# Performance work log

Measured on AMD Instinct MI355X. Metric: run time of the kernel, lower is better.

The kernel has to match this reference:

```python
import jax, jax.numpy as jnp
import numpy as np

SHIFT = 1
EPS = 1e-5

def setup_inputs() -> dict:
    key = jax.random.key(0)
    k1, k2, k3, k4, k5, k6 = jax.random.split(key, 6)
    B, C, H, Wd = 64, 512, 28, 28
    Cout = 512
    return {
        "x": jax.random.normal(k1, (B, C, H, Wd), dtype=jnp.float32),
        "W": jax.random.normal(k2, (Cout, C), dtype=jnp.float32) * 0.05,
        "gamma": jax.random.uniform(k3, (Cout,), dtype=jnp.float32) + 0.5,
        "beta": jax.random.normal(k4, (Cout,), dtype=jnp.float32) * 0.1,
        "running_mean": jax.random.normal(k5, (Cout,), dtype=jnp.float32) * 0.1,
        "running_var": jax.random.uniform(k6, (Cout,), dtype=jnp.float32) + 0.5,
    }

def reference(x, W, gamma, beta, running_mean, running_var):
    # Group-wise spatial shift: split channels into 4 groups, roll each.
    Cg = x.shape[1] // 4
    x1 = jnp.roll(x[:, 0*Cg:1*Cg], -SHIFT, axis=2)  # up
    x2 = jnp.roll(x[:, 1*Cg:2*Cg],  SHIFT, axis=2)  # down
    x3 = jnp.roll(x[:, 2*Cg:3*Cg], -SHIFT, axis=3)  # left
    x4 = jnp.roll(x[:, 3*Cg:4*Cg],  SHIFT, axis=3)  # right
    shifted = jnp.concatenate([x1, x2, x3, x4], axis=1)  # [B,C,H,W]
    # 1x1 conv (no bias) == channel matmul
    y = jnp.einsum('bchw,oc->bohw', shifted, W)
    # BatchNorm (inference: running stats) folded to scale/shift, then ReLU
    scale = gamma * jax.lax.rsqrt(running_var + EPS)
    shift = beta - running_mean * scale
    y = y * scale[None, :, None, None] + shift[None, :, None, None]
    return jnp.maximum(y, 0.0)
```

## Files before the change

kernel.cpp:

```cpp
#include <hip/hip_runtime.h>

#define BN   64
#define CIN  512
#define COUT 512
#define HW   784
#define NT   128
#define MT   112
#define BK   64
#define NKB  (CIN / BK)

typedef __attribute__((ext_vector_type(8))) short short8;
typedef __attribute__((ext_vector_type(4))) float f32x4;

__device__ __forceinline__ unsigned short f2bf(float f) {
    union { float f; unsigned int u; } v; v.f = f;
    unsigned int r = v.u + 0x7fffu + ((v.u >> 16) & 1u);
    return (unsigned short)(r >> 16);
}

__device__ __forceinline__ uint2 pack4(float a, float b, float c, float d) {
    uint2 r;
    r.x = (unsigned int)f2bf(a) | ((unsigned int)f2bf(b) << 16);
    r.y = (unsigned int)f2bf(c) | ((unsigned int)f2bf(d) << 16);
    return r;
}

__global__ __launch_bounds__(256)
void p0_wcvt(const float* __restrict__ W, unsigned short* __restrict__ Wb)
{
    int gi = blockIdx.x * 256 + threadIdx.x;
    const float* p = W + (size_t)gi * 8;
    float4 a = *(const float4*)p;
    float4 c = *(const float4*)(p + 4);
    uint2 lo = pack4(a.x, a.y, a.z, a.w);
    uint2 hi = pack4(c.x, c.y, c.z, c.w);
    uint4 v; v.x = lo.x; v.y = lo.y; v.z = hi.x; v.w = hi.y;
    *(uint4*)(Wb + (size_t)gi * 8) = v;
}

__global__ __launch_bounds__(512, 2)
void p_fused(const float* __restrict__ x, const unsigned short* __restrict__ Wb,
             const float* __restrict__ gamma, const float* __restrict__ beta,
             const float* __restrict__ rmean, const float* __restrict__ rvar,
             float* __restrict__ out)
{
    __shared__ unsigned short sX[2][MT * BK];

    const int t  = threadIdx.x;
    const int id = blockIdx.x;
    const int mt = id % 7;
    const int b  = id / 7;
    const int hw_base = mt * MT;
    const int lane = t & 63, wv = t >> 6, m16 = lane & 15, q = lane >> 4;
    const float* xb = x + (size_t)b * CIN * HW;

    const int cq = t & 15;
    const int mq = t >> 4;
    const bool act = (mq < 28);
    const int hw = hw_base + mq * 4;
    const int h  = hw / 28;
    const int w0 = hw - h * 28;

    float4 va0, va1, va2, va3;
    float  ex0, ex1, ex2, ex3;

    auto loadx = [&](int kk) {
        if (!act) return;
        const int g = kk >> 1;
        const float* src = xb + (size_t)(kk * BK + cq * 4) * HW;
        if (g < 2) {
            int shw = hw + (g == 0 ? 28 : HW - 28);
            if (shw >= HW) shw -= HW;
            va0 = *(const float4*)(src + 0 * HW + shw);
            va1 = *(const float4*)(src + 1 * HW + shw);
            va2 = *(const float4*)(src + 2 * HW + shw);
            va3 = *(const float4*)(src + 3 * HW + shw);
        } else {
            const int base = h * 28;
            const int wx = (g == 2) ? ((w0 + 4 < 28) ? (w0 + 4) : 0)
                                    : ((w0 == 0) ? 27 : (w0 - 1));
            const float* r0 = src + 0 * HW + base;
            const float* r1 = src + 1 * HW + base;
            const float* r2 = src + 2 * HW + base;
            const float* r3 = src + 3 * HW + base;
            va0 = *(const float4*)(r0 + w0);  ex0 = r0[wx];
            va1 = *(const float4*)(r1 + w0);  ex1 = r1[wx];
            va2 = *(const float4*)(r2 + w0);  ex2 = r2[wx];
            va3 = *(const float4*)(r3 + w0);  ex3 = r3[wx];
        }
    };

    auto packst = [&](int kk, unsigned short* buf) {
        if (!act) return;
        const int g = kk >> 1;
        float4 r0 = va0, r1 = va1, r2 = va2, r3 = va3;
        if (g == 2) {
            r0 = make_float4(va0.y, va0.z, va0.w, ex0);
            r1 = make_float4(va1.y, va1.z, va1.w, ex1);
            r2 = make_float4(va2.y, va2.z, va2.w, ex2);
            r3 = make_float4(va3.y, va3.z, va3.w, ex3);
        } else if (g == 3) {
            r0 = make_float4(ex0, va0.x, va0.y, va0.z);
            r1 = make_float4(ex1, va1.x, va1.y, va1.z);
            r2 = make_float4(ex2, va2.x, va2.y, va2.z);
            r3 = make_float4(ex3, va3.x, va3.y, va3.z);
        }
        uint2 u0 = pack4(r0.x, r1.x, r2.x, r3.x);
        uint2 u1 = pack4(r0.y, r1.y, r2.y, r3.y);
        uint2 u2 = pack4(r0.z, r1.z, r2.z, r3.z);
        uint2 u3 = pack4(r0.w, r1.w, r2.w, r3.w);
        const int m0 = mq * 4;
        const int gr = cq >> 1, hf4 = (cq & 1) * 4;
        *(uint2*)(&buf[(m0 + 0) * BK + ((gr ^ ((m0 + 0) & 7)) * 8) + hf4]) = u0;
        *(uint2*)(&buf[(m0 + 1) * BK + ((gr ^ ((m0 + 1) & 7)) * 8) + hf4]) = u1;
        *(uint2*)(&buf[(m0 + 2) * BK + ((gr ^ ((m0 + 2) & 7)) * 8) + hf4]) = u2;
        *(uint2*)(&buf[(m0 + 3) * BK + ((gr ^ ((m0 + 3) & 7)) * 8) + hf4]) = u3;
    };

    const unsigned short* wr0 = Wb + (size_t)(wv * 64 + m16) * CIN + q * 8;
    const unsigned short* wr1 = wr0 + 16 * CIN;
    const unsigned short* wr2 = wr0 + 32 * CIN;
    const unsigned short* wr3 = wr0 + 48 * CIN;

    short8 wc[2][4], wn[2][4];
#define LOADW(DST, KK)                                  \
    {   const int ko = (KK) * 64;                       \
        DST[0][0] = *(const short8*)(wr0 + ko);         \
        DST[0][1] = *(const short8*)(wr1 + ko);         \
        DST[0][2] = *(const short8*)(wr2 + ko);         \
        DST[0][3] = *(const short8*)(wr3 + ko);         \
        DST[1][0] = *(const short8*)(wr0 + ko + 32);    \
        DST[1][1] = *(const short8*)(wr1 + ko + 32);    \
        DST[1][2] = *(const short8*)(wr2 + ko + 32);    \
        DST[1][3] = *(const short8*)(wr3 + ko + 32);    \
    }

    f32x4 acc[4][7];
    #pragma unroll
    for (int i = 0; i < 4; ++i)
        #pragma unroll
        for (int j = 0; j < 7; ++j)
            acc[i][j] = (f32x4){0.f, 0.f, 0.f, 0.f};

#define COMPUTE(XS, WF)                                                          \
    {                                                                            \
        const unsigned short* xs = (XS);                                         \
        _Pragma("unroll")                                                        \
        for (int ks = 0; ks < 2; ++ks) {                                         \
            _Pragma("unroll")                                                    \
            for (int bm = 0; bm < 7; ++bm) {                                     \
                int m  = bm * 16 + m16;                                          \
                int sl = (ks * 4 + q) ^ (m & 7);                                 \
                short8 bf = *(const short8*)(&xs[m * BK + sl * 8]);              \
                acc[0][bm] = __builtin_amdgcn_mfma_f32_16x16x32_bf16(WF[ks][0], bf, acc[0][bm], 0, 0, 0); \
                acc[1][bm] = __builtin_amdgcn_mfma_f32_16x16x32_bf16(WF[ks][1], bf, acc[1][bm], 0, 0, 0); \
                acc[2][bm] = __builtin_amdgcn_mfma_f32_16x16x32_bf16(WF[ks][2], bf, acc[2][bm], 0, 0, 0); \
                acc[3][bm] = __builtin_amdgcn_mfma_f32_16x16x32_bf16(WF[ks][3], bf, acc[3][bm], 0, 0, 0); \
            }                                                                    \
        }                                                                        \
    }

    loadx(0);
    LOADW(wc, 0);
    packst(0, sX[0]);
    __syncthreads();

    #pragma unroll 1
    for (int kp = 0; kp < 4; ++kp) {
        {
            const int kn = 2 * kp + 1;
            loadx(kn);
            LOADW(wn, kn);
            COMPUTE(sX[0], wc);
            packst(kn, sX[1]);
            __syncthreads();
        }
        {
            const int kn = 2 * kp + 2;
            if (kn < NKB) {
                loadx(kn);
                LOADW(wc, kn);
            }
            COMPUTE(sX[1], wn);
            if (kn < NKB) {
                packst(kn, sX[0]);
            }
            __syncthreads();
        }
    }
#undef COMPUTE
#undef LOADW

    float scl[4][4], shf[4][4];
    #pragma unroll
    for (int bo = 0; bo < 4; ++bo)
        #pragma unroll
        for (int r = 0; r < 4; ++r) {
            int o = wv * 64 + bo * 16 + q * 4 + r;
            float sc = gamma[o] * rsqrtf(rvar[o] + 1e-5f);
            scl[bo][r] = sc;
            shf[bo][r] = beta[o] - rmean[o] * sc;
        }
    float* outb = out + (size_t)b * COUT * HW;
    #pragma unroll
    for (int bo = 0; bo < 4; ++bo) {
        #pragma unroll
        for (int r = 0; r < 4; ++r) {
            int o = wv * 64 + bo * 16 + q * 4 + r;
            float* orow = outb + (size_t)o * HW + hw_base + m16;
            #pragma unroll
            for (int bm = 0; bm < 7; ++bm) {
                float y = acc[bo][bm][r] * scl[bo][r] + shf[bo][r];
                y = fmaxf(y, 0.f);
                __builtin_nontemporal_store(y, orow + bm * 16);
            }
        }
    }
}

#define SW_STRIDE 72
#define SX_STRIDE 64
__global__ __launch_bounds__(256, 2)
void shiftconv_fallback(const float* __restrict__ x, const float* __restrict__ Wf,
                        const float* __restrict__ gamma, const float* __restrict__ beta,
                        const float* __restrict__ rmean, const float* __restrict__ rvar,
                        float* __restrict__ out)
{
    __shared__ unsigned short sW[NT * SW_STRIDE];
    __shared__ unsigned short sX[MT * SX_STRIDE];
    const int t = threadIdx.x;
    const int ot = blockIdx.x, mt = blockIdx.y, b = blockIdx.z;
    const int o_base = ot * NT, hw_base = mt * MT;
    const float* xb = x + (size_t)b * CIN * HW;
    const int lane = t & 63, wv = t >> 6, m16 = lane & 15, q = lane >> 4;
    f32x4 acc[2][7];
    #pragma unroll
    for (int i = 0; i < 2; ++i)
        #pragma unroll
        for (int j = 0; j < 7; ++j) acc[i][j] = (f32x4){0.f, 0.f, 0.f, 0.f};
    #pragma unroll
    for (int kk = 0; kk < CIN / BK; ++kk) {
        const int k0 = kk * BK;
        const int g = k0 >> 7;
        #pragma unroll
        for (int e0 = 0; e0 < 2; ++e0) {
            int e = t + e0 * 256;
            if (e < (BK / 4) * (MT / 4)) {
                int cq = e / 28, mq = e - cq * 28;
                int hw = hw_base + mq * 4;
                const float* src = xb + (size_t)(k0 + cq * 4) * HW;
                float4 v0, v1, v2, v3;
                if (g < 2) {
                    int shw = hw + (g == 0 ? 28 : HW - 28);
                    if (shw >= HW) shw -= HW;
                    v0 = *(const float4*)(src + 0 * HW + shw);
                    v1 = *(const float4*)(src + 1 * HW + shw);
                    v2 = *(const float4*)(src + 2 * HW + shw);
                    v3 = *(const float4*)(src + 3 * HW + shw);
                } else {
                    int h = hw / 28, w0 = hw - h * 28, base = h * 28;
                    #pragma unroll
                    for (int j = 0; j < 4; ++j) {
                        const float* row = src + j * HW + base;
                        float4 a = *(const float4*)(row + w0);
                        float4 r;
                        if (g == 2) {
                            float ex = row[(w0 + 4 < 28) ? (w0 + 4) : 0];
                            r.x = a.y; r.y = a.z; r.z = a.w; r.w = ex;
                        } else {
                            float ex = row[(w0 == 0) ? 27 : (w0 - 1)];
                            r.x = ex; r.y = a.x; r.z = a.y; r.w = a.z;
                        }
                        if (j == 0) v0 = r; else if (j == 1) v1 = r;
                        else if (j == 2) v2 = r; else v3 = r;
                    }
                }
                int m0 = mq * 4;
                { int p = (cq + 5 * (m0 + 0)) & 15;
                  *(uint2*)(&sX[(m0 + 0) * SX_STRIDE + p * 4]) = pack4(v0.x, v1.x, v2.x, v3.x); }
                { int p = (cq + 5 * (m0 + 1)) & 15;
                  *(uint2*)(&sX[(m0 + 1) * SX_STRIDE + p * 4]) = pack4(v0.y, v1.y, v2.y, v3.y); }
                { int p = (cq + 5 * (m0 + 2)) & 15;
                  *(uint2*)(&sX[(m0 + 2) * SX_STRIDE + p * 4]) = pack4(v0.z, v1.z, v2.z, v3.z); }
                { int p = (cq + 5 * (m0 + 3)) & 15;
                  *(uint2*)(&sX[(m0 + 3) * SX_STRIDE + p * 4]) = pack4(v0.w, v1.w, v2.w, v3.w); }
            }
        }
        #pragma unroll
        for (int i = 0; i < 4; ++i) {
            int e = t + i * 256;
            int ol = e >> 3, kg = (e & 7) * 8;
            const float* wr = Wf + (size_t)(o_base + ol) * CIN + k0 + kg;
            float4 a = *(const float4*)(wr);
            float4 c = *(const float4*)(wr + 4);
            uint2 lo = pack4(a.x, a.y, a.z, a.w);
            uint2 hi = pack4(c.x, c.y, c.z, c.w);
            uint4 v; v.x = lo.x; v.y = lo.y; v.z = hi.x; v.w = hi.y;
            *(uint4*)(&sW[ol * SW_STRIDE + kg]) = v;
        }
        __syncthreads();
        #pragma unroll
        for (int ks = 0; ks < BK; ks += 32) {
            short8 afrag[2];
            #pragma unroll
            for (int bo = 0; bo < 2; ++bo) {
                int row = wv * 32 + bo * 16 + m16;
                afrag[bo] = *(const short8*)(&sW[row * SW_STRIDE + ks + q * 8]);
            }
            #pragma unroll
            for (int bm = 0; bm < 7; ++bm) {
                int m = bm * 16 + m16;
                int g0 = (ks >> 2) + 2 * q;
                int p0 = (g0 + 5 * m) & 15;
                int p1 = (g0 + 1 + 5 * m) & 15;
                uint2 lo = *(const uint2*)(&sX[m * SX_STRIDE + p0 * 4]);
                uint2 hi = *(const uint2*)(&sX[m * SX_STRIDE + p1 * 4]);
                union { uint2 u2[2]; short8 s; } fb;
                fb.u2[0] = lo; fb.u2[1] = hi;
                acc[0][bm] = __builtin_amdgcn_mfma_f32_16x16x32_bf16(afrag[0], fb.s, acc[0][bm], 0, 0, 0);
                acc[1][bm] = __builtin_amdgcn_mfma_f32_16x16x32_bf16(afrag[1], fb.s, acc[1][bm], 0, 0, 0);
            }
        }
        __syncthreads();
    }
    float scl[2][4], shf[2][4];
    #pragma unroll
    for (int bo = 0; bo < 2; ++bo)
        #pragma unroll
        for (int r = 0; r < 4; ++r) {
            int o = o_base + wv * 32 + bo * 16 + q * 4 + r;
            float sc = gamma[o] * rsqrtf(rvar[o] + 1e-5f);
            scl[bo][r] = sc;
            shf[bo][r] = beta[o] - rmean[o] * sc;
        }
    float* outb = out + (size_t)b * COUT * HW;
    #pragma unroll
    for (int bo = 0; bo < 2; ++bo)
        #pragma unroll
        for (int r = 0; r < 4; ++r) {
            int o = o_base + wv * 32 + bo * 16 + q * 4 + r;
            float* orow = outb + (size_t)o * HW + hw_base + m16;
            #pragma unroll
            for (int bm = 0; bm < 7; ++bm) {
                float y = acc[bo][bm][r] * scl[bo][r] + shf[bo][r];
                y = fmaxf(y, 0.f);
                __builtin_nontemporal_store(y, orow + bm * 16);
            }
        }
}

extern "C" void kernel_launch(void* const* d_in, const int* in_sizes, int n_in,
                              void* d_out, int out_size, void* d_ws, size_t ws_size,
                              hipStream_t stream)
{
    const float* x     = (const float*)d_in[0];
    const float* W     = (const float*)d_in[1];
    const float* gamma = (const float*)d_in[2];
    const float* beta  = (const float*)d_in[3];
    const float* rmean = (const float*)d_in[4];
    const float* rvar  = (const float*)d_in[5];
    float* out = (float*)d_out;

    const size_t wb_bytes = (size_t)COUT * CIN * 2;
    if (ws_size >= wb_bytes) {
        unsigned short* Wb = (unsigned short*)d_ws;
        p0_wcvt<<<dim3(128), dim3(256), 0, stream>>>(W, Wb);
        p_fused<<<dim3(448), dim3(512), 0, stream>>>(x, Wb, gamma, beta, rmean, rvar, out);
    } else {
        dim3 grid(COUT / NT, HW / MT, BN);
        shiftconv_fallback<<<grid, 256, 0, stream>>>(x, W, gamma, beta, rmean, rvar, out);
    }
}
```

Baseline: 237.2 us.

## Split output channels across 4 blocks with 256 threads for more occupancy

Each block now computes a 128-output-channel slice instead of all 512, with 256 threads per block and a 1792-block grid. Block IDs are swizzled so the four channel-tile blocks of one (batch, spatial) pair launch adjacently and can share the x tile in L2. Each thread now loads two x row groups, and the per-wave accumulator footprint halves, which allows 3 blocks per CU. The cost is that the shifted x tile is loaded from global memory and converted to bf16 four times instead of once.

```diff
diff --git a/kernel.cpp b/kernel.cpp
--- a/kernel.cpp
+++ b/kernel.cpp
@@ -38,7 +38,9 @@
     *(uint4*)(Wb + (size_t)gi * 8) = v;
 }
 
-__global__ __launch_bounds__(512, 2)
+struct XR { float4 v0, v1, v2, v3; float e0, e1, e2, e3; };
+
+__global__ __launch_bounds__(256, 3)
 void p_fused(const float* __restrict__ x, const unsigned short* __restrict__ Wb,
              const float* __restrict__ gamma, const float* __restrict__ beta,
              const float* __restrict__ rmean, const float* __restrict__ rvar,
@@ -47,34 +49,37 @@
     __shared__ unsigned short sX[2][MT * BK];
 
     const int t  = threadIdx.x;
-    const int id = blockIdx.x;
-    const int mt = id % 7;
-    const int b  = id / 7;
+    const int id   = blockIdx.x;
+    const int ot   = (id >> 3) & 3;
+    const int pair = ((id >> 5) << 3) | (id & 7);
+    const int mt   = pair % 7;
+    const int b    = pair / 7;
+    const int o_base  = ot * NT;
     const int hw_base = mt * MT;
     const int lane = t & 63, wv = t >> 6, m16 = lane & 15, q = lane >> 4;
     const float* xb = x + (size_t)b * CIN * HW;
 
-    const int cq = t & 15;
-    const int mq = t >> 4;
-    const bool act = (mq < 28);
-    const int hw = hw_base + mq * 4;
-    const int h  = hw / 28;
-    const int w0 = hw - h * 28;
-
-    float4 va0, va1, va2, va3;
-    float  ex0, ex1, ex2, ex3;
-
-    auto loadx = [&](int kk) {
-        if (!act) return;
+    const int cq  = t & 15;
+    const int mqA = t >> 4;
+    const int mqB = mqA + 16;
+    const bool actB = (mqB < 28);
+    const int hwA = hw_base + mqA * 4;
+    const int hA  = hwA / 28,  wA = hwA - hA * 28;
+    const int hwB = hw_base + mqB * 4;
+    const int hB  = hwB / 28,  wB = hwB - hB * 28;
+
+    XR ra, rb;
+
+    auto loadx = [&](int kk, int hw, int h, int w0, XR& r) {
         const int g = kk >> 1;
         const float* src = xb + (size_t)(kk * BK + cq * 4) * HW;
         if (g < 2) {
             int shw = hw + (g == 0 ? 28 : HW - 28);
             if (shw >= HW) shw -= HW;
-            va0 = *(const float4*)(src + 0 * HW + shw);
-            va1 = *(const float4*)(src + 1 * HW + shw);
-            va2 = *(const float4*)(src + 2 * HW + shw);
-            va3 = *(const float4*)(src + 3 * HW + shw);
+            r.v0 = *(const float4*)(src + 0 * HW + shw);
+            r.v1 = *(const float4*)(src + 1 * HW + shw);
+            r.v2 = *(const float4*)(src + 2 * HW + shw);
+            r.v3 = *(const float4*)(src + 3 * HW + shw);
         } else {
             const int base = h * 28;
             const int wx = (g == 2) ? ((w0 + 4 < 28) ? (w0 + 4) : 0)
@@ -83,27 +88,26 @@
             const float* r1 = src + 1 * HW + base;
             const float* r2 = src + 2 * HW + base;
             const float* r3 = src + 3 * HW + base;
-            va0 = *(const float4*)(r0 + w0);  ex0 = r0[wx];
-            va1 = *(const float4*)(r1 + w0);  ex1 = r1[wx];
-            va2 = *(const float4*)(r2 + w0);  ex2 = r2[wx];
-            va3 = *(const float4*)(r3 + w0);  ex3 = r3[wx];
+            r.v0 = *(const float4*)(r0 + w0);  r.e0 = r0[wx];
+            r.v1 = *(const float4*)(r1 + w0);  r.e1 = r1[wx];
+            r.v2 = *(const float4*)(r2 + w0);  r.e2 = r2[wx];
+            r.v3 = *(const float4*)(r3 + w0);  r.e3 = r3[wx];
         }
     };
 
-    auto packst = [&](int kk, unsigned short* buf) {
-        if (!act) return;
+    auto packst = [&](int kk, int mq, const XR& r, unsigned short* buf) {
         const int g = kk >> 1;
-        float4 r0 = va0, r1 = va1, r2 = va2, r3 = va3;
+        float4 r0 = r.v0, r1 = r.v1, r2 = r.v2, r3 = r.v3;
         if (g == 2) {
-            r0 = make_float4(va0.y, va0.z, va0.w, ex0);
-            r1 = make_float4(va1.y, va1.z, va1.w, ex1);
-            r2 = make_float4(va2.y, va2.z, va2.w, ex2);
-            r3 = make_float4(va3.y, va3.z, va3.w, ex3);
+            r0 = make_float4(r.v0.y, r.v0.z, r.v0.w, r.e0);
+            r1 = make_float4(r.v1.y, r.v1.z, r.v1.w, r.e1);
+            r2 = make_float4(r.v2.y, r.v2.z, r.v2.w, r.e2);
+            r3 = make_float4(r.v3.y, r.v3.z, r.v3.w, r.e3);
         } else if (g == 3) {
-            r0 = make_float4(ex0, va0.x, va0.y, va0.z);
-            r1 = make_float4(ex1, va1.x, va1.y, va1.z);
-            r2 = make_float4(ex2, va2.x, va2.y, va2.z);
-            r3 = make_float4(ex3, va3.x, va3.y, va3.z);
+            r0 = make_float4(r.e0, r.v0.x, r.v0.y, r.v0.z);
+            r1 = make_float4(r.e1, r.v1.x, r.v1.y, r.v1.z);
+            r2 = make_float4(r.e2, r.v2.x, r.v2.y, r.v2.z);
+            r3 = make_float4(r.e3, r.v3.x, r.v3.y, r.v3.z);
         }
         uint2 u0 = pack4(r0.x, r1.x, r2.x, r3.x);
         uint2 u1 = pack4(r0.y, r1.y, r2.y, r3.y);
@@ -117,27 +121,21 @@
         *(uint2*)(&buf[(m0 + 3) * BK + ((gr ^ ((m0 + 3) & 7)) * 8) + hf4]) = u3;
     };
 
-    const unsigned short* wr0 = Wb + (size_t)(wv * 64 + m16) * CIN + q * 8;
+    const unsigned short* wr0 = Wb + (size_t)(o_base + wv * 32 + m16) * CIN + q * 8;
     const unsigned short* wr1 = wr0 + 16 * CIN;
-    const unsigned short* wr2 = wr0 + 32 * CIN;
-    const unsigned short* wr3 = wr0 + 48 * CIN;
-
-    short8 wc[2][4], wn[2][4];
+
+    short8 wc[2][2], wn[2][2];
 #define LOADW(DST, KK)                                  \
     {   const int ko = (KK) * 64;                       \
         DST[0][0] = *(const short8*)(wr0 + ko);         \
         DST[0][1] = *(const short8*)(wr1 + ko);         \
-        DST[0][2] = *(const short8*)(wr2 + ko);         \
-        DST[0][3] = *(const short8*)(wr3 + ko);         \
         DST[1][0] = *(const short8*)(wr0 + ko + 32);    \
         DST[1][1] = *(const short8*)(wr1 + ko + 32);    \
-        DST[1][2] = *(const short8*)(wr2 + ko + 32);    \
-        DST[1][3] = *(const short8*)(wr3 + ko + 32);    \
-    }
-
-    f32x4 acc[4][7];
-    #pragma unroll
-    for (int i = 0; i < 4; ++i)
+    }
+
+    f32x4 acc[2][7];
+    #pragma unroll
+    for (int i = 0; i < 2; ++i)
         #pragma unroll
         for (int j = 0; j < 7; ++j)
             acc[i][j] = (f32x4){0.f, 0.f, 0.f, 0.f};
@@ -154,36 +152,40 @@
                 short8 bf = *(const short8*)(&xs[m * BK + sl * 8]);              \
                 acc[0][bm] = __builtin_amdgcn_mfma_f32_16x16x32_bf16(WF[ks][0], bf, acc[0][bm], 0, 0, 0); \
                 acc[1][bm] = __builtin_amdgcn_mfma_f32_16x16x32_bf16(WF[ks][1], bf, acc[1][bm], 0, 0, 0); \
-                acc[2][bm] = __builtin_amdgcn_mfma_f32_16x16x32_bf16(WF[ks][2], bf, acc[2][bm], 0, 0, 0); \
-                acc[3][bm] = __builtin_amdgcn_mfma_f32_16x16x32_bf16(WF[ks][3], bf, acc[3][bm], 0, 0, 0); \
             }                                                                    \
         }                                                                        \
     }
 
-    loadx(0);
+    loadx(0, hwA, hA, wA, ra);
+    if (actB) loadx(0, hwB, hB, wB, rb);
     LOADW(wc, 0);
-    packst(0, sX[0]);
+    packst(0, mqA, ra, sX[0]);
+    if (actB) packst(0, mqB, rb, sX[0]);
     __syncthreads();
 
     #pragma unroll 1
     for (int kp = 0; kp < 4; ++kp) {
         {
             const int kn = 2 * kp + 1;
-            loadx(kn);
+            loadx(kn, hwA, hA, wA, ra);
+            if (actB) loadx(kn, hwB, hB, wB, rb);
             LOADW(wn, kn);
             COMPUTE(sX[0], wc);
-            packst(kn, sX[1]);
+            packst(kn, mqA, ra, sX[1]);
+            if (actB) packst(kn, mqB, rb, sX[1]);
             __syncthreads();
         }
         {
             const int kn = 2 * kp + 2;
             if (kn < NKB) {
-                loadx(kn);
+                loadx(kn, hwA, hA, wA, ra);
+                if (actB) loadx(kn, hwB, hB, wB, rb);
                 LOADW(wc, kn);
             }
             COMPUTE(sX[1], wn);
             if (kn < NKB) {
-                packst(kn, sX[0]);
+                packst(kn, mqA, ra, sX[0]);
+                if (actB) packst(kn, mqB, rb, sX[0]);
             }
             __syncthreads();
         }
@@ -191,22 +193,22 @@
 #undef COMPUTE
 #undef LOADW
 
-    float scl[4][4], shf[4][4];
-    #pragma unroll
-    for (int bo = 0; bo < 4; ++bo)
+    float scl[2][4], shf[2][4];
+    #pragma unroll
+    for (int bo = 0; bo < 2; ++bo)
         #pragma unroll
         for (int r = 0; r < 4; ++r) {
-            int o = wv * 64 + bo * 16 + q * 4 + r;
+            int o = o_base + wv * 32 + bo * 16 + q * 4 + r;
             float sc = gamma[o] * rsqrtf(rvar[o] + 1e-5f);
             scl[bo][r] = sc;
             shf[bo][r] = beta[o] - rmean[o] * sc;
         }
     float* outb = out + (size_t)b * COUT * HW;
     #pragma unroll
-    for (int bo = 0; bo < 4; ++bo) {
+    for (int bo = 0; bo < 2; ++bo) {
         #pragma unroll
         for (int r = 0; r < 4; ++r) {
-            int o = wv * 64 + bo * 16 + q * 4 + r;
+            int o = o_base + wv * 32 + bo * 16 + q * 4 + r;
             float* orow = outb + (size_t)o * HW + hw_base + m16;
             #pragma unroll
             for (int bm = 0; bm < 7; ++bm) {
@@ -365,7 +367,7 @@
     if (ws_size >= wb_bytes) {
         unsigned short* Wb = (unsigned short*)d_ws;
         p0_wcvt<<<dim3(128), dim3(256), 0, stream>>>(W, Wb);
-        p_fused<<<dim3(448), dim3(512), 0, stream>>>(x, Wb, gamma, beta, rmean, rvar, out);
+        p_fused<<<dim3(1792), dim3(256), 0, stream>>>(x, Wb, gamma, beta, rmean, rvar, out);
     } else {
         dim3 grid(COUT / NT, HW / MT, BN);
         shiftconv_fallback<<<grid, 256, 0, stream>>>(x, W, gamma, beta, rmean, rvar, out);
```

Result: slower. 328.9 us (+38.6%).

## Stage all eight K-slices of shifted x in LDS and cut barriers to two

Applied to the files above, without the earlier changes.

The LDS tile becomes a full K buffer (8 slices instead of a double buffer). Slices 0–3 are loaded and packed up front. Slices 4–7 are loaded and packed while slices 0–3 are multiplied, so only two block barriers remain instead of one per K slice. Weight fragments are now loaded inside each phase rather than prefetched one step ahead. The cost is about 112KB of LDS per block, which likely stops two blocks sharing a CU and may push the 448 blocks into a second wave.

```diff
diff --git a/kernel.cpp b/kernel.cpp
--- a/kernel.cpp
+++ b/kernel.cpp
@@ -38,13 +38,15 @@
     *(uint4*)(Wb + (size_t)gi * 8) = v;
 }
 
+struct XR { float4 v0, v1, v2, v3; float e0, e1, e2, e3; };
+
 __global__ __launch_bounds__(512, 2)
 void p_fused(const float* __restrict__ x, const unsigned short* __restrict__ Wb,
              const float* __restrict__ gamma, const float* __restrict__ beta,
              const float* __restrict__ rmean, const float* __restrict__ rvar,
              float* __restrict__ out)
 {
-    __shared__ unsigned short sX[2][MT * BK];
+    __shared__ unsigned short sX[NKB][MT * BK];
 
     const int t  = threadIdx.x;
     const int id = blockIdx.x;
@@ -61,20 +63,18 @@
     const int h  = hw / 28;
     const int w0 = hw - h * 28;
 
-    float4 va0, va1, va2, va3;
-    float  ex0, ex1, ex2, ex3;
-
-    auto loadx = [&](int kk) {
-        if (!act) return;
+    XR ra, rb;
+
+    auto loadx = [&](int kk, XR& r) {
         const int g = kk >> 1;
         const float* src = xb + (size_t)(kk * BK + cq * 4) * HW;
         if (g < 2) {
             int shw = hw + (g == 0 ? 28 : HW - 28);
             if (shw >= HW) shw -= HW;
-            va0 = *(const float4*)(src + 0 * HW + shw);
-            va1 = *(const float4*)(src + 1 * HW + shw);
-            va2 = *(const float4*)(src + 2 * HW + shw);
-            va3 = *(const float4*)(src + 3 * HW + shw);
+            r.v0 = *(const float4*)(src + 0 * HW + shw);
+            r.v1 = *(const float4*)(src + 1 * HW + shw);
+            r.v2 = *(const float4*)(src + 2 * HW + shw);
+            r.v3 = *(const float4*)(src + 3 * HW + shw);
         } else {
             const int base = h * 28;
             const int wx = (g == 2) ? ((w0 + 4 < 28) ? (w0 + 4) : 0)
@@ -83,27 +83,26 @@
             const float* r1 = src + 1 * HW + base;
             const float* r2 = src + 2 * HW + base;
             const float* r3 = src + 3 * HW + base;
-            va0 = *(const float4*)(r0 + w0);  ex0 = r0[wx];
-            va1 = *(const float4*)(r1 + w0);  ex1 = r1[wx];
-            va2 = *(const float4*)(r2 + w0);  ex2 = r2[wx];
-            va3 = *(const float4*)(r3 + w0);  ex3 = r3[wx];
+            r.v0 = *(const float4*)(r0 + w0);  r.e0 = r0[wx];
+            r.v1 = *(const float4*)(r1 + w0);  r.e1 = r1[wx];
+            r.v2 = *(const float4*)(r2 + w0);  r.e2 = r2[wx];
+            r.v3 = *(const float4*)(r3 + w0);  r.e3 = r3[wx];
         }
     };
 
-    auto packst = [&](int kk, unsigned short* buf) {
-        if (!act) return;
+    auto packst = [&](int kk, const XR& r, unsigned short* buf) {
         const int g = kk >> 1;
-        float4 r0 = va0, r1 = va1, r2 = va2, r3 = va3;
+        float4 r0 = r.v0, r1 = r.v1, r2 = r.v2, r3 = r.v3;
         if (g == 2) {
-            r0 = make_float4(va0.y, va0.z, va0.w, ex0);
-            r1 = make_float4(va1.y, va1.z, va1.w, ex1);
-            r2 = make_float4(va2.y, va2.z, va2.w, ex2);
-            r3 = make_float4(va3.y, va3.z, va3.w, ex3);
+            r0 = make_float4(r.v0.y, r.v0.z, r.v0.w, r.e0);
+            r1 = make_float4(r.v1.y, r.v1.z, r.v1.w, r.e1);
+            r2 = make_float4(r.v2.y, r.v2.z, r.v2.w, r.e2);
+            r3 = make_float4(r.v3.y, r.v3.z, r.v3.w, r.e3);
         } else if (g == 3) {
-            r0 = make_float4(ex0, va0.x, va0.y, va0.z);
-            r1 = make_float4(ex1, va1.x, va1.y, va1.z);
-            r2 = make_float4(ex2, va2.x, va2.y, va2.z);
-            r3 = make_float4(ex3, va3.x, va3.y, va3.z);
+            r0 = make_float4(r.e0, r.v0.x, r.v0.y, r.v0.z);
+            r1 = make_float4(r.e1, r.v1.x, r.v1.y, r.v1.z);
+            r2 = make_float4(r.e2, r.v2.x, r.v2.y, r.v2.z);
+            r3 = make_float4(r.e3, r.v3.x, r.v3.y, r.v3.z);
         }
         uint2 u0 = pack4(r0.x, r1.x, r2.x, r3.x);
         uint2 u1 = pack4(r0.y, r1.y, r2.y, r3.y);
@@ -122,19 +121,6 @@
     const unsigned short* wr2 = wr0 + 32 * CIN;
     const unsigned short* wr3 = wr0 + 48 * CIN;
 
-    short8 wc[2][4], wn[2][4];
-#define LOADW(DST, KK)                                  \
-    {   const int ko = (KK) * 64;                       \
-        DST[0][0] = *(const short8*)(wr0 + ko);         \
-        DST[0][1] = *(const short8*)(wr1 + ko);         \
-        DST[0][2] = *(const short8*)(wr2 + ko);         \
-        DST[0][3] = *(const short8*)(wr3 + ko);         \
-        DST[1][0] = *(const short8*)(wr0 + ko + 32);    \
-        DST[1][1] = *(const short8*)(wr1 + ko + 32);    \
-        DST[1][2] = *(const short8*)(wr2 + ko + 32);    \
-        DST[1][3] = *(const short8*)(wr3 + ko + 32);    \
-    }
-
     f32x4 acc[4][7];
     #pragma unroll
     for (int i = 0; i < 4; ++i)
@@ -142,54 +128,77 @@
         for (int j = 0; j < 7; ++j)
             acc[i][j] = (f32x4){0.f, 0.f, 0.f, 0.f};
 
-#define COMPUTE(XS, WF)                                                          \
+#define MFMA16(A, B, C) __builtin_amdgcn_mfma_f32_16x16x32_bf16((A), (B), (C), 0, 0, 0)
+#define PHASE(KK, XS)                                                            \
     {                                                                            \
+        const int ko = (KK) * 64;                                                \
+        short8 wf0 = *(const short8*)(wr0 + ko);                                 \
+        short8 wf1 = *(const short8*)(wr1 + ko);                                 \
+        short8 wf2 = *(const short8*)(wr2 + ko);                                 \
+        short8 wf3 = *(const short8*)(wr3 + ko);                                 \
+        short8 wg0 = *(const short8*)(wr0 + ko + 32);                            \
+        short8 wg1 = *(const short8*)(wr1 + ko + 32);                            \
+        short8 wg2 = *(const short8*)(wr2 + ko + 32);                            \
+        short8 wg3 = *(const short8*)(wr3 + ko + 32);                            \
         const unsigned short* xs = (XS);                                         \
         _Pragma("unroll")                                                        \
-        for (int ks = 0; ks < 2; ++ks) {                                         \
-            _Pragma("unroll")                                                    \
-            for (int bm = 0; bm < 7; ++bm) {                                     \
-                int m  = bm * 16 + m16;                                          \
-                int sl = (ks * 4 + q) ^ (m & 7);                                 \
-                short8 bf = *(const short8*)(&xs[m * BK + sl * 8]);              \
-                acc[0][bm] = __builtin_amdgcn_mfma_f32_16x16x32_bf16(WF[ks][0], bf, acc[0][bm], 0, 0, 0); \
-                acc[1][bm] = __builtin_amdgcn_mfma_f32_16x16x32_bf16(WF[ks][1], bf, acc[1][bm], 0, 0, 0); \
-                acc[2][bm] = __builtin_amdgcn_mfma_f32_16x16x32_bf16(WF[ks][2], bf, acc[2][bm], 0, 0, 0); \
-                acc[3][bm] = __builtin_amdgcn_mfma_f32_16x16x32_bf16(WF[ks][3], bf, acc[3][bm], 0, 0, 0); \
-            }                                                                    \
+        for (int bm = 0; bm < 7; ++bm) {                                         \
+            int m   = bm * 16 + m16;                                             \
+            int sl0 = q ^ (m & 7);                                               \
+            int sl1 = (4 + q) ^ (m & 7);                                         \
+            short8 bf0 = *(const short8*)(&xs[m * BK + sl0 * 8]);                \
+            short8 bf1 = *(const short8*)(&xs[m * BK + sl1 * 8]);                \
+            acc[0][bm] = MFMA16(wf0, bf0, acc[0][bm]);                           \
+            acc[1][bm] = MFMA16(wf1, bf0, acc[1][bm]);                           \
+            acc[2][bm] = MFMA16(wf2, bf0, acc[2][bm]);                           \
+            acc[3][bm] = MFMA16(wf3, bf0, acc[3][bm]);                           \
+            acc[0][bm] = MFMA16(wg0, bf1, acc[0][bm]);                           \
+            acc[1][bm] = MFMA16(wg1, bf1, acc[1][bm]);                           \
+            acc[2][bm] = MFMA16(wg2, bf1, acc[2][bm]);                           \
+            acc[3][bm] = MFMA16(wg3, bf1, acc[3][bm]);                           \
         }                                                                        \
     }
 
-    loadx(0);
-    LOADW(wc, 0);
-    packst(0, sX[0]);
+    if (act) {
+        loadx(0, ra);
+        loadx(1, rb);
+        packst(0, ra, sX[0]);
+        loadx(2, ra);
+        packst(1, rb, sX[1]);
+        loadx(3, rb);
+        packst(2, ra, sX[2]);
+        packst(3, rb, sX[3]);
+    }
     __syncthreads();
 
-    #pragma unroll 1
-    for (int kp = 0; kp < 4; ++kp) {
-        {
-            const int kn = 2 * kp + 1;
-            loadx(kn);
-            LOADW(wn, kn);
-            COMPUTE(sX[0], wc);
-            packst(kn, sX[1]);
-            __syncthreads();
-        }
-        {
-            const int kn = 2 * kp + 2;
-            if (kn < NKB) {
-                loadx(kn);
-                LOADW(wc, kn);
-            }
-            COMPUTE(sX[1], wn);
-            if (kn < NKB) {
-                packst(kn, sX[0]);
-            }
-            __syncthreads();
-        }
-    }
-#undef COMPUTE
-#undef LOADW
+    if (act) loadx(4, ra);
+    {
+        if (act) loadx(5, rb);
+        PHASE(0, sX[0]);
+        if (act) packst(4, ra, sX[4]);
+    }
+    {
+        if (act) loadx(6, ra);
+        PHASE(1, sX[1]);
+        if (act) packst(5, rb, sX[5]);
+    }
+    {
+        if (act) loadx(7, rb);
+        PHASE(2, sX[2]);
+        if (act) packst(6, ra, sX[6]);
+    }
+    {
+        PHASE(3, sX[3]);
+        if (act) packst(7, rb, sX[7]);
+    }
+    __syncthreads();
+
+    PHASE(4, sX[4]);
+    PHASE(5, sX[5]);
+    PHASE(6, sX[6]);
+    PHASE(7, sX[7]);
+#undef PHASE
+#undef MFMA16
 
     float scl[4][4], shf[4][4];
     #pragma unroll
```

Result: no change. 235.3 us (-0.8%).

## Stage x tiles via global_load_lds into fp32 LDS, then transpose-pack to bf16

Applied to the files above, without the earlier changes.

Replaces per-thread register loads of shifted x with direct global-to-LDS DMA (global_load_lds) into an fp32 staging buffer with swizzled layout. A separate TRANS step reads from LDS, applies the W-axis shift, converts to bf16 and writes the MFMA operand tile. This drops the double-buffered bf16 tile in favour of one fp32 staging buffer plus one bf16 buffer. It also remaps block IDs for locality and raises the launch-bounds occupancy hint. The aim is to cut register pressure and global load instruction overhead, at the cost of an extra LDS round trip and an extra barrier per k-step.

```diff
diff --git a/kernel.cpp b/kernel.cpp
--- a/kernel.cpp
+++ b/kernel.cpp
@@ -23,6 +23,13 @@
     r.x = (unsigned int)f2bf(a) | ((unsigned int)f2bf(b) << 16);
     r.y = (unsigned int)f2bf(c) | ((unsigned int)f2bf(d) << 16);
     return r;
+}
+
+__device__ __forceinline__ void gl_lds16(const float* g, unsigned short* l) {
+    __builtin_amdgcn_global_load_lds(
+        (const __attribute__((address_space(1))) unsigned int*)g,
+        (__attribute__((address_space(3))) unsigned int*)l,
+        16, 0, 0);
 }
 
 __global__ __launch_bounds__(256)
@@ -38,72 +45,83 @@
     *(uint4*)(Wb + (size_t)gi * 8) = v;
 }
 
-__global__ __launch_bounds__(512, 2)
+__global__ __launch_bounds__(512, 6)
 void p_fused(const float* __restrict__ x, const unsigned short* __restrict__ Wb,
              const float* __restrict__ gamma, const float* __restrict__ beta,
              const float* __restrict__ rmean, const float* __restrict__ rvar,
              float* __restrict__ out)
 {
-    __shared__ unsigned short sX[2][MT * BK];
+    __shared__ float sR[64 * 128];
+    __shared__ unsigned short sB[MT * BK];
 
     const int t  = threadIdx.x;
-    const int id = blockIdx.x;
+    const int id = (blockIdx.x & 7) * 56 + (blockIdx.x >> 3);
     const int mt = id % 7;
     const int b  = id / 7;
     const int hw_base = mt * MT;
     const int lane = t & 63, wv = t >> 6, m16 = lane & 15, q = lane >> 4;
     const float* xb = x + (size_t)b * CIN * HW;
+    unsigned short* sR16 = (unsigned short*)sR;
 
     const int cq = t & 15;
     const int mq = t >> 4;
     const bool act = (mq < 28);
-    const int hw = hw_base + mq * 4;
-    const int h  = hw / 28;
-    const int w0 = hw - h * 28;
-
-    float4 va0, va1, va2, va3;
-    float  ex0, ex1, ex2, ex3;
-
-    auto loadx = [&](int kk) {
+
+    auto STAGE = [&](int kk) {
+        const int g = kk >> 1;
+        #pragma unroll
+        for (int i = 0; i < 4; ++i) {
+            const int gr_ = i * 512 + t;
+            const int c   = gr_ >> 5;
+            const int jp  = gr_ & 31;
+            const int jl  = (jp & 24) | ((jp & 7) ^ ((c >> 2) & 7));
+            const float* crow = xb + (size_t)(kk * BK + c) * HW;
+            const float* src;
+            if (jl < 28) {
+                int hw0 = hw_base + jl * 4;
+                if (g == 0) { hw0 += 28; if (hw0 >= HW) hw0 -= HW; }
+                else if (g == 1) { hw0 -= 28; if (hw0 < 0) hw0 += HW; }
+                src = crow + hw0;
+            } else {
+                src = crow + hw_base;
+            }
+            const int gbase = i * 512 + (t & ~63);
+            gl_lds16(src, sR16 + (size_t)gbase * 8);
+        }
+    };
+
+    auto TRANS = [&](int kk) {
         if (!act) return;
-        const int g = kk >> 1;
-        const float* src = xb + (size_t)(kk * BK + cq * 4) * HW;
-        if (g < 2) {
-            int shw = hw + (g == 0 ? 28 : HW - 28);
-            if (shw >= HW) shw -= HW;
-            va0 = *(const float4*)(src + 0 * HW + shw);
-            va1 = *(const float4*)(src + 1 * HW + shw);
-            va2 = *(const float4*)(src + 2 * HW + shw);
-            va3 = *(const float4*)(src + 3 * HW + shw);
-        } else {
-            const int base = h * 28;
-            const int wx = (g == 2) ? ((w0 + 4 < 28) ? (w0 + 4) : 0)
-                                    : ((w0 == 0) ? 27 : (w0 - 1));
-            const float* r0 = src + 0 * HW + base;
-            const float* r1 = src + 1 * HW + base;
-            const float* r2 = src + 2 * HW + base;
-            const float* r3 = src + 3 * HW + base;
-            va0 = *(const float4*)(r0 + w0);  ex0 = r0[wx];
-            va1 = *(const float4*)(r1 + w0);  ex1 = r1[wx];
-            va2 = *(const float4*)(r2 + w0);  ex2 = r2[wx];
-            va3 = *(const float4*)(r3 + w0);  ex3 = r3[wx];
-        }
-    };
-
-    auto packst = [&](int kk, unsigned short* buf) {
-        if (!act) return;
-        const int g = kk >> 1;
-        float4 r0 = va0, r1 = va1, r2 = va2, r3 = va3;
-        if (g == 2) {
-            r0 = make_float4(va0.y, va0.z, va0.w, ex0);
-            r1 = make_float4(va1.y, va1.z, va1.w, ex1);
-            r2 = make_float4(va2.y, va2.z, va2.w, ex2);
-            r3 = make_float4(va3.y, va3.z, va3.w, ex3);
-        } else if (g == 3) {
-            r0 = make_float4(ex0, va0.x, va0.y, va0.z);
-            r1 = make_float4(ex1, va1.x, va1.y, va1.z);
-            r2 = make_float4(ex2, va2.x, va2.y, va2.z);
-            r3 = make_float4(ex3, va3.x, va3.y, va3.z);
+        const int g  = kk >> 1;
+        const int sg = cq & 7;
+        const int p  = (mq & 24) | ((mq & 7) ^ sg);
+        const int c0 = cq * 4;
+        float4 a0 = *(const float4*)&sR[(c0 + 0) * 128 + p * 4];
+        float4 a1 = *(const float4*)&sR[(c0 + 1) * 128 + p * 4];
+        float4 a2 = *(const float4*)&sR[(c0 + 2) * 128 + p * 4];
+        float4 a3 = *(const float4*)&sR[(c0 + 3) * 128 + p * 4];
+        float4 r0 = a0, r1 = a1, r2 = a2, r3 = a3;
+        if (g >= 2) {
+            const int m7 = mq % 7;
+            const int nb = (g == 2) ? ((m7 == 6) ? mq - 6 : mq + 1)
+                                    : ((m7 == 0) ? mq + 6 : mq - 1);
+            const int np = (nb & 24) | ((nb & 7) ^ sg);
+            const int so = (g == 2) ? 0 : 3;
+            float e0 = sR[(c0 + 0) * 128 + np * 4 + so];
+            float e1 = sR[(c0 + 1) * 128 + np * 4 + so];
+            float e2 = sR[(c0 + 2) * 128 + np * 4 + so];
+            float e3 = sR[(c0 + 3) * 128 + np * 4 + so];
+            if (g == 2) {
+                r0 = make_float4(a0.y, a0.z, a0.w, e0);
+                r1 = make_float4(a1.y, a1.z, a1.w, e1);
+                r2 = make_float4(a2.y, a2.z, a2.w, e2);
+                r3 = make_float4(a3.y, a3.z, a3.w, e3);
+            } else {
+                r0 = make_float4(e0, a0.x, a0.y, a0.z);
+                r1 = make_float4(e1, a1.x, a1.y, a1.z);
+                r2 = make_float4(e2, a2.x, a2.y, a2.z);
+                r3 = make_float4(e3, a3.x, a3.y, a3.z);
+            }
         }
         uint2 u0 = pack4(r0.x, r1.x, r2.x, r3.x);
         uint2 u1 = pack4(r0.y, r1.y, r2.y, r3.y);
@@ -111,10 +129,10 @@
         uint2 u3 = pack4(r0.w, r1.w, r2.w, r3.w);
         const int m0 = mq * 4;
         const int gr = cq >> 1, hf4 = (cq & 1) * 4;
-        *(uint2*)(&buf[(m0 + 0) * BK + ((gr ^ ((m0 + 0) & 7)) * 8) + hf4]) = u0;
-        *(uint2*)(&buf[(m0 + 1) * BK + ((gr ^ ((m0 + 1) & 7)) * 8) + hf4]) = u1;
-        *(uint2*)(&buf[(m0 + 2) * BK + ((gr ^ ((m0 + 2) & 7)) * 8) + hf4]) = u2;
-        *(uint2*)(&buf[(m0 + 3) * BK + ((gr ^ ((m0 + 3) & 7)) * 8) + hf4]) = u3;
+        *(uint2*)(&sB[(m0 + 0) * BK + ((gr ^ ((m0 + 0) & 7)) * 8) + hf4]) = u0;
+        *(uint2*)(&sB[(m0 + 1) * BK + ((gr ^ ((m0 + 1) & 7)) * 8) + hf4]) = u1;
+        *(uint2*)(&sB[(m0 + 2) * BK + ((gr ^ ((m0 + 2) & 7)) * 8) + hf4]) = u2;
+        *(uint2*)(&sB[(m0 + 3) * BK + ((gr ^ ((m0 + 3) & 7)) * 8) + hf4]) = u3;
     };
 
     const unsigned short* wr0 = Wb + (size_t)(wv * 64 + m16) * CIN + q * 8;
@@ -122,17 +140,17 @@
     const unsigned short* wr2 = wr0 + 32 * CIN;
     const unsigned short* wr3 = wr0 + 48 * CIN;
 
-    short8 wc[2][4], wn[2][4];
+    short8 wA[8], wB[8];
 #define LOADW(DST, KK)                                  \
     {   const int ko = (KK) * 64;                       \
-        DST[0][0] = *(const short8*)(wr0 + ko);         \
-        DST[0][1] = *(const short8*)(wr1 + ko);         \
-        DST[0][2] = *(const short8*)(wr2 + ko);         \
-        DST[0][3] = *(const short8*)(wr3 + ko);         \
-        DST[1][0] = *(const short8*)(wr0 + ko + 32);    \
-        DST[1][1] = *(const short8*)(wr1 + ko + 32);    \
-        DST[1][2] = *(const short8*)(wr2 + ko + 32);    \
-        DST[1][3] = *(const short8*)(wr3 + ko + 32);    \
+        DST[0] = *(const short8*)(wr0 + ko);            \
+        DST[1] = *(const short8*)(wr1 + ko);            \
+        DST[2] = *(const short8*)(wr2 + ko);            \
+        DST[3] = *(const short8*)(wr3 + ko);            \
+        DST[4] = *(const short8*)(wr0 + ko + 32);       \
+        DST[5] = *(const short8*)(wr1 + ko + 32);       \
+        DST[6] = *(const short8*)(wr2 + ko + 32);       \
+        DST[7] = *(const short8*)(wr3 + ko + 32);       \
     }
 
     f32x4 acc[4][7];
@@ -142,53 +160,56 @@
         for (int j = 0; j < 7; ++j)
             acc[i][j] = (f32x4){0.f, 0.f, 0.f, 0.f};
 
-#define COMPUTE(XS, WF)                                                          \
+#define MFMA16(A, B, C) __builtin_amdgcn_mfma_f32_16x16x32_bf16((A), (B), (C), 0, 0, 0)
+#define COMPUTE(WF)                                                              \
     {                                                                            \
-        const unsigned short* xs = (XS);                                         \
         _Pragma("unroll")                                                        \
-        for (int ks = 0; ks < 2; ++ks) {                                         \
-            _Pragma("unroll")                                                    \
-            for (int bm = 0; bm < 7; ++bm) {                                     \
-                int m  = bm * 16 + m16;                                          \
-                int sl = (ks * 4 + q) ^ (m & 7);                                 \
-                short8 bf = *(const short8*)(&xs[m * BK + sl * 8]);              \
-                acc[0][bm] = __builtin_amdgcn_mfma_f32_16x16x32_bf16(WF[ks][0], bf, acc[0][bm], 0, 0, 0); \
-                acc[1][bm] = __builtin_amdgcn_mfma_f32_16x16x32_bf16(WF[ks][1], bf, acc[1][bm], 0, 0, 0); \
-                acc[2][bm] = __builtin_amdgcn_mfma_f32_16x16x32_bf16(WF[ks][2], bf, acc[2][bm], 0, 0, 0); \
-                acc[3][bm] = __builtin_amdgcn_mfma_f32_16x16x32_bf16(WF[ks][3], bf, acc[3][bm], 0, 0, 0); \
-            }                                                                    \
+        for (int bm = 0; bm < 7; ++bm) {                                         \
+            int m   = bm * 16 + m16;                                             \
+            int sl0 = q ^ (m & 7);                                               \
+            int sl1 = (4 + q) ^ (m & 7);                                         \
+            short8 bf0 = *(const short8*)(&sB[m * BK + sl0 * 8]);                \
+            short8 bf1 = *(const short8*)(&sB[m * BK + sl1 * 8]);                \
+            acc[0][bm] = MFMA16(WF[0], bf0, acc[0][bm]);                         \
+            acc[1][bm] = MFMA16(WF[1], bf0, acc[1][bm]);                         \
+            acc[2][bm] = MFMA16(WF[2], bf0, acc[2][bm]);                         \
+            acc[3][bm] = MFMA16(WF[3], bf0, acc[3][bm]);                         \
+            acc[0][bm] = MFMA16(WF[4], bf1, acc[0][bm]);                         \
+            acc[1][bm] = MFMA16(WF[5], bf1, acc[1][bm]);                         \
+            acc[2][bm] = MFMA16(WF[6], bf1, acc[2][bm]);                         \
+            acc[3][bm] = MFMA16(WF[7], bf1, acc[3][bm]);                         \
         }                                                                        \
     }
 
-    loadx(0);
-    LOADW(wc, 0);
-    packst(0, sX[0]);
+    STAGE(0);
+    LOADW(wA, 0);
     __syncthreads();
 
-    #pragma unroll 1
-    for (int kp = 0; kp < 4; ++kp) {
-        {
-            const int kn = 2 * kp + 1;
-            loadx(kn);
-            LOADW(wn, kn);
-            COMPUTE(sX[0], wc);
-            packst(kn, sX[1]);
-            __syncthreads();
-        }
-        {
-            const int kn = 2 * kp + 2;
-            if (kn < NKB) {
-                loadx(kn);
-                LOADW(wc, kn);
-            }
-            COMPUTE(sX[1], wn);
-            if (kn < NKB) {
-                packst(kn, sX[0]);
-            }
-            __syncthreads();
-        }
-    }
+#define PHASE_E(KK)                           \
+    TRANS(KK);                                                                   \
+    __syncthreads();                                                             \
+    if ((KK) < 7) { STAGE((KK) + 1); LOADW(wB, (KK) + 1); }                      \
+    COMPUTE(wA);                                                                 \
+    if ((KK) < 7) __syncthreads();
+#define PHASE_O(KK)                            \
+    TRANS(KK);                                                                   \
+    __syncthreads();                                                             \
+    if ((KK) < 7) { STAGE((KK) + 1); LOADW(wA, (KK) + 1); }                      \
+    COMPUTE(wB);                                                                 \
+    if ((KK) < 7) __syncthreads();
+
+    PHASE_E(0)
+    PHASE_O(1)
+    PHASE_E(2)
+    PHASE_O(3)
+    PHASE_E(4)
+    PHASE_O(5)
+    PHASE_E(6)
+    PHASE_O(7)
+#undef PHASE_E
+#undef PHASE_O
 #undef COMPUTE
+#undef MFMA16
 #undef LOADW
 
     float scl[4][4], shf[4][4];
```

New measurement: 665.0 us. 2.8x slower.
